# Kernel optimization log

Hardware: AMD Instinct MI355X
Metric: run time of the kernel (lower is better)

The kernel has to match this reference:

```python
import jax, jax.numpy as jnp
import numpy as np
from jax import lax

B, T, I, H = 64, 2048, 64, 256


def setup_inputs() -> dict:
    key = jax.random.key(0)
    ks = jax.random.split(key, 7)
    s = 1.0 / np.sqrt(H)  # PyTorch LSTM/Linear init scale
    x = jax.random.normal(ks[0], (B, T, I), dtype=jnp.float32)
    W_ih = jax.random.uniform(ks[1], (4 * H, I), minval=-s, maxval=s, dtype=jnp.float32)
    W_hh = jax.random.uniform(ks[2], (4 * H, H), minval=-s, maxval=s, dtype=jnp.float32)
    b_ih = jax.random.uniform(ks[3], (4 * H,), minval=-s, maxval=s, dtype=jnp.float32)
    b_hh = jax.random.uniform(ks[4], (4 * H,), minval=-s, maxval=s, dtype=jnp.float32)
    W_o = jax.random.uniform(ks[5], (1, H), minval=-s, maxval=s, dtype=jnp.float32)
    b_o = jax.random.uniform(ks[6], (1,), minval=-s, maxval=s, dtype=jnp.float32)
    return {"x": x, "W_ih": W_ih, "W_hh": W_hh, "b_ih": b_ih, "b_hh": b_hh, "W_o": W_o, "b_o": b_o}


def _lstm(x, W_ih, W_hh, b_ih, b_hh):
    # x: [B, T, I]. PyTorch gate order: i, f, g, o.
    Bn, Tn, _ = x.shape
    Hn = W_hh.shape[1]
    # Precompute input contribution for all timesteps (one big GEMM).
    gx = jnp.einsum('bti,gi->btg', x, W_ih) + b_ih + b_hh  # [B, T, 4H]

    def step(carry, gxt):
        h, c = carry
        gates = gxt + h @ W_hh.T  # [B, 4H]
        i, f, g, o = jnp.split(gates, 4, axis=-1)
        c = jax.nn.sigmoid(f) * c + jax.nn.sigmoid(i) * jnp.tanh(g)
        h = jax.nn.sigmoid(o) * jnp.tanh(c)
        return (h, c), h

    h0 = jnp.zeros((Bn, Hn), x.dtype)
    (_, _), hs = lax.scan(step, (h0, h0), jnp.swapaxes(gx, 0, 1))  # hs: [T, B, H]
    return jnp.swapaxes(hs, 0, 1)  # [B, T, H]


def reference(x, W_ih, W_hh, b_ih, b_hh, W_o, b_o):
    hs = _lstm(x, W_ih, W_hh, b_ih, b_hh)          # [B, T, H]
    return hs @ W_o.T + b_o                         # [B, T, 1]
```

## Files before the change

kernel.cpp:

```cpp
#include <hip/hip_runtime.h>
#include <hip/hip_fp16.h>

#define B_  64
#define T_  2048
#define I_  64
#define H_  256
#define G4_ 1024

typedef _Float16 h2v __attribute__((ext_vector_type(2)));

__device__ __forceinline__ float fdot2(uint32_t a, uint32_t b, float c) {
#if __has_builtin(__builtin_amdgcn_fdot2)
    return __builtin_amdgcn_fdot2(__builtin_bit_cast(h2v, a), __builtin_bit_cast(h2v, b), c, false);
#else
    h2v ha = __builtin_bit_cast(h2v, a), hb = __builtin_bit_cast(h2v, b);
    return c + (float)ha.x * (float)hb.x + (float)ha.y * (float)hb.y;
#endif
}

__device__ __forceinline__ ushort f2h(float v) {
    return __builtin_bit_cast(ushort, (_Float16)v);
}
__device__ __forceinline__ float h2f(ushort v) {
    return (float)__builtin_bit_cast(_Float16, v);
}

__global__ void repack_kernel(const float* __restrict__ Whh, ushort* __restrict__ wpk) {
    int o  = blockIdx.x * 256 + threadIdx.x;
    int j  = o & 7;
    int h  = (o >> 3) & 255;
    int kc = (o >> 11) & 31;
    int g  = o >> 16;
    float v = Whh[(g * 256 + h) * 256 + kc * 8 + j];
    wpk[o] = f2h(v);
}

__global__ __launch_bounds__(256) void gx_kernel(
    const float* __restrict__ x, const float* __restrict__ Wih,
    const float* __restrict__ bih, const float* __restrict__ bhh,
    ushort* __restrict__ gx2, int t0, int TCc) {

    __shared__ uint32_t xsp[32][32];
    const int bt0 = blockIdx.x * 32;
    const int gq  = blockIdx.y;
    const int row = gq * 256 + threadIdx.x;

    for (int i = threadIdx.x; i < 512; i += 256) {
        int r  = i >> 4, c4 = i & 15;
        int bt = bt0 + r;
        int b  = bt / TCc;
        int tl = bt - b * TCc;
        float4 v = *(const float4*)(&x[(((size_t)b * T_) + t0 + tl) * I_ + c4 * 4]);
        xsp[r][c4 * 2 + 0] = (uint32_t)f2h(v.x) | ((uint32_t)f2h(v.y) << 16);
        xsp[r][c4 * 2 + 1] = (uint32_t)f2h(v.z) | ((uint32_t)f2h(v.w) << 16);
    }
    __syncthreads();

    uint32_t wp[32];
#pragma unroll
    for (int k = 0; k < 32; ++k) {
        float a = Wih[row * I_ + 2 * k];
        float b = Wih[row * I_ + 2 * k + 1];
        wp[k] = (uint32_t)f2h(a) | ((uint32_t)f2h(b) << 16);
    }
    const float bias = bih[row] + bhh[row];

    for (int i = 0; i < 32; ++i) {
        float acc = bias;
#pragma unroll
        for (int k4 = 0; k4 < 8; ++k4) {
            uint4 xq = *(const uint4*)(&xsp[i][k4 * 4]);
            acc = fdot2(wp[k4 * 4 + 0], xq.x, acc);
            acc = fdot2(wp[k4 * 4 + 1], xq.y, acc);
            acc = fdot2(wp[k4 * 4 + 2], xq.z, acc);
            acc = fdot2(wp[k4 * 4 + 3], xq.w, acc);
        }
        gx2[((size_t)(bt0 + i) * 256 + threadIdx.x) * 4 + gq] = f2h(acc);
    }
}

__global__ __launch_bounds__(512, 1)
void lstm_kernel(
    const ushort* __restrict__ wpk, const ushort* __restrict__ gx2,
    ushort* __restrict__ hbuf,
    float* __restrict__ state,
    int TCc, int t0, int first) {

    __shared__ __align__(16) ushort wg4[14 * 2 * 256 * 8];
    __shared__ __align__(16) ushort hs[256];
    __shared__ __align__(16) float pex[256][4];

    const int tid   = threadIdx.x;
    const int hd    = tid & 255;
    const int q     = tid >> 8;
    const int kbase = q << 4;
    const int b     = blockIdx.x;
    const bool q0   = (q == 0);

    uint32_t wi[64], wf[64], wg[64];
#pragma unroll
    for (int k = 0; k < 16; ++k) {
        uint4 v = *(const uint4*)(wpk + (size_t)(0 * 32 + kbase + k) * 2048 + hd * 8);
        wi[k * 4 + 0] = v.x; wi[k * 4 + 1] = v.y; wi[k * 4 + 2] = v.z; wi[k * 4 + 3] = v.w;
    }
#pragma unroll
    for (int k = 0; k < 16; ++k) {
        uint4 v = *(const uint4*)(wpk + (size_t)(1 * 32 + kbase + k) * 2048 + hd * 8);
        wf[k * 4 + 0] = v.x; wf[k * 4 + 1] = v.y; wf[k * 4 + 2] = v.z; wf[k * 4 + 3] = v.w;
    }
#pragma unroll
    for (int k = 0; k < 16; ++k) {
        uint4 v = *(const uint4*)(wpk + (size_t)(2 * 32 + kbase + k) * 2048 + hd * 8);
        wg[k * 4 + 0] = v.x; wg[k * 4 + 1] = v.y; wg[k * 4 + 2] = v.z; wg[k * 4 + 3] = v.w;
    }
#pragma unroll
    for (int k = 0; k < 14; ++k) {
        uint4 v = *(const uint4*)(wpk + (size_t)(3 * 32 + kbase + k) * 2048 + hd * 8);
        *(uint4*)(wg4 + ((k * 2 + q) * 256 + hd) * 8) = v;
    }
    uint32_t wo_r[8];
#pragma unroll
    for (int k = 0; k < 2; ++k) {
        uint4 v = *(const uint4*)(wpk + (size_t)(3 * 32 + kbase + 14 + k) * 2048 + hd * 8);
        wo_r[k * 4 + 0] = v.x; wo_r[k * 4 + 1] = v.y; wo_r[k * 4 + 2] = v.z; wo_r[k * 4 + 3] = v.w;
    }

    float c = 0.f, h = 0.f;
    if (q0) {
        if (!first) {
            c = state[b * H_ + hd];
            h = state[B_ * H_ + b * H_ + hd];
        }
        hs[hd] = f2h(h);
    }
    __syncthreads();

    const ushort* gxb = gx2 + (size_t)b * TCc * G4_;
    ushort* hb = hbuf + (size_t)b * T_ * H_ + (size_t)t0 * H_;

    ushort4 cg;
    if (q0) cg = *(const ushort4*)(gxb + (size_t)0 * G4_ + hd * 4);

    for (int tl = 0; tl < TCc; ++tl) {
        ushort4 ng;
        if (q0) {
            const int tn = (tl + 1 < TCc) ? tl + 1 : tl;
            ng = *(const ushort4*)(gxb + (size_t)tn * G4_ + hd * 4);
        }

        float ai = 0.f, af = 0.f, agv = 0.f, ao = 0.f;

#pragma unroll
        for (int k = 0; k < 14; ++k) {
            const int kc = kbase + k;
            uint4 hq = *(const uint4*)(hs + kc * 8);
            uint4 wo = *(const uint4*)(wg4 + ((k * 2 + q) * 256 + hd) * 8);
            ai  = fdot2(wi[k * 4 + 0], hq.x, ai);
            ai  = fdot2(wi[k * 4 + 1], hq.y, ai);
            ai  = fdot2(wi[k * 4 + 2], hq.z, ai);
            ai  = fdot2(wi[k * 4 + 3], hq.w, ai);
            af  = fdot2(wf[k * 4 + 0], hq.x, af);
            af  = fdot2(wf[k * 4 + 1], hq.y, af);
            af  = fdot2(wf[k * 4 + 2], hq.z, af);
            af  = fdot2(wf[k * 4 + 3], hq.w, af);
            agv = fdot2(wg[k * 4 + 0], hq.x, agv);
            agv = fdot2(wg[k * 4 + 1], hq.y, agv);
            agv = fdot2(wg[k * 4 + 2], hq.z, agv);
            agv = fdot2(wg[k * 4 + 3], hq.w, agv);
            ao  = fdot2(wo.x, hq.x, ao);
            ao  = fdot2(wo.y, hq.y, ao);
            ao  = fdot2(wo.z, hq.z, ao);
            ao  = fdot2(wo.w, hq.w, ao);
        }
#pragma unroll
        for (int k = 14; k < 16; ++k) {
            const int kc = kbase + k;
            const int r  = (k - 14) * 4;
            uint4 hq = *(const uint4*)(hs + kc * 8);
            ai  = fdot2(wi[k * 4 + 0], hq.x, ai);
            ai  = fdot2(wi[k * 4 + 1], hq.y, ai);
            ai  = fdot2(wi[k * 4 + 2], hq.z, ai);
            ai  = fdot2(wi[k * 4 + 3], hq.w, ai);
            af  = fdot2(wf[k * 4 + 0], hq.x, af);
            af  = fdot2(wf[k * 4 + 1], hq.y, af);
            af  = fdot2(wf[k * 4 + 2], hq.z, af);
            af  = fdot2(wf[k * 4 + 3], hq.w, af);
            agv = fdot2(wg[k * 4 + 0], hq.x, agv);
            agv = fdot2(wg[k * 4 + 1], hq.y, agv);
            agv = fdot2(wg[k * 4 + 2], hq.z, agv);
            agv = fdot2(wg[k * 4 + 3], hq.w, agv);
            ao  = fdot2(wo_r[r + 0], hq.x, ao);
            ao  = fdot2(wo_r[r + 1], hq.y, ao);
            ao  = fdot2(wo_r[r + 2], hq.z, ao);
            ao  = fdot2(wo_r[r + 3], hq.w, ao);
        }

        if (!q0) {
            float4 p; p.x = ai; p.y = af; p.z = agv; p.w = ao;
            *(float4*)(&pex[hd][0]) = p;
        }
        __syncthreads();

        if (q0) {
            float4 px = *(const float4*)(&pex[hd][0]);
            ai += px.x; af += px.y; agv += px.z; ao += px.w;

            ai += h2f(cg.x); af += h2f(cg.y); agv += h2f(cg.z); ao += h2f(cg.w);

            float si = __builtin_amdgcn_rcpf(1.f + __expf(-ai));
            float sf = __builtin_amdgcn_rcpf(1.f + __expf(-af));
            float so = __builtin_amdgcn_rcpf(1.f + __expf(-ao));
            float eg = __expf(2.f * agv);
            float tg = (eg - 1.f) * __builtin_amdgcn_rcpf(eg + 1.f);
            c = sf * c + si * tg;
            float ec = __expf(2.f * c);
            float tc = (ec - 1.f) * __builtin_amdgcn_rcpf(ec + 1.f);
            h = so * tc;

            ushort hh = f2h(h);
            hs[hd] = hh;
            hb[(size_t)tl * H_ + hd] = hh;
            cg = ng;
        }
        __syncthreads();
    }

    if (q0) {
        state[b * H_ + hd]           = c;
        state[B_ * H_ + b * H_ + hd] = h;
    }
}

__global__ __launch_bounds__(256) void proj_kernel(
    const ushort* __restrict__ hbuf, const float* __restrict__ Wo,
    const float* __restrict__ bo, float* __restrict__ out) {

    const int lane = threadIdx.x & 63;
    const int wid  = blockIdx.x * 4 + (threadIdx.x >> 6);
    const int nw   = gridDim.x * 4;
    const int rows = B_ * T_;

    float4 w = *(const float4*)(Wo + lane * 4);
    const float bov = bo[0];

    for (int r = wid; r < rows; r += nw) {
        const ushort* hp = hbuf + (size_t)r * H_ + lane * 4;
        ushort4 u = *(const ushort4*)hp;
        float p = h2f(u.x) * w.x + h2f(u.y) * w.y + h2f(u.z) * w.z + h2f(u.w) * w.w;
#pragma unroll
        for (int m = 1; m < 64; m <<= 1) p += __shfl_xor(p, m, 64);
        if (lane == 0) out[r] = p + bov;
    }
}

extern "C" void kernel_launch(void* const* d_in, const int* in_sizes, int n_in,
                              void* d_out, int out_size, void* d_ws, size_t ws_size,
                              hipStream_t stream) {
    const float* x   = (const float*)d_in[0];
    const float* Wih = (const float*)d_in[1];
    const float* Whh = (const float*)d_in[2];
    const float* bih = (const float*)d_in[3];
    const float* bhh = (const float*)d_in[4];
    const float* Wo  = (const float*)d_in[5];
    const float* bo  = (const float*)d_in[6];
    float* out = (float*)d_out;

    char* ws = (char*)d_ws;
    ushort* wpk   = (ushort*)ws;
    float*  state = (float*)(ws + 512 * 1024);
    ushort* hbuf  = (ushort*)(ws + 640 * 1024);
    const size_t hbuf_bytes = (size_t)B_ * T_ * H_ * 2;
    char*   dyn   = ws + 640 * 1024 + hbuf_bytes;

    size_t fixed = 640 * 1024 + hbuf_bytes;
    size_t avail = (ws_size > fixed) ? ws_size - fixed : 0;
    long long tcmax = (long long)(avail / ((size_t)B_ * G4_ * 2));
    int TC = (tcmax > 512) ? 512 : (int)tcmax;
    TC &= ~63;
    if (TC < 64) TC = 64;

    repack_kernel<<<1024, 256, 0, stream>>>(Whh, wpk);

    for (int t0 = 0; t0 < T_; t0 += TC) {
        int TCc = (T_ - t0 < TC) ? (T_ - t0) : TC;
        ushort* gxb = (ushort*)dyn;
        dim3 g1((B_ * TCc) / 32, 4);
        gx_kernel<<<g1, 256, 0, stream>>>(x, Wih, bih, bhh, gxb, t0, TCc);
        lstm_kernel<<<B_, 512, 0, stream>>>(wpk, gxb, hbuf, state, TCc, t0, t0 == 0 ? 1 : 0);
    }
    proj_kernel<<<512, 256, 0, stream>>>(hbuf, Wo, bo, out);
    (void)in_sizes; (void)n_in; (void)out_size;
}
```

Before: 3.123 ms.

## Split LSTM gates across two workgroups per batch with global-memory flag handshake

Each batch row is now handled by two workgroups (128 total), each computing two of the four gate matvecs with weights fully in registers, which removes the shared-memory weight tile for the fourth gate. Partial gate sums are exchanged every timestep through global memory, using double-buffered slots and release/acquire flag spinning between the paired blocks. This halves per-step FMA work per block and spreads the recurrence over more CUs. In exchange it adds a cross-CU round trip through L2 on every step and relies on both paired blocks being co-resident, otherwise the spin-wait can deadlock.

New measurement: 10.12 ms. 224% more time.

```diff
diff --git a/kernel.cpp b/kernel.cpp
--- a/kernel.cpp
+++ b/kernel.cpp
@@ -84,45 +84,33 @@
     const ushort* __restrict__ wpk, const ushort* __restrict__ gx2,
     ushort* __restrict__ hbuf,
     float* __restrict__ state,
+    unsigned* __restrict__ flags,
+    unsigned long long* __restrict__ parts,
     int TCc, int t0, int first) {
 
-    __shared__ __align__(16) ushort wg4[14 * 2 * 256 * 8];
     __shared__ __align__(16) ushort hs[256];
-    __shared__ __align__(16) float pex[256][4];
+    __shared__ __align__(16) float pex[256][2];
 
     const int tid   = threadIdx.x;
     const int hd    = tid & 255;
     const int q     = tid >> 8;
     const int kbase = q << 4;
-    const int b     = blockIdx.x;
+    const int role  = blockIdx.x >> 6;
+    const int b     = blockIdx.x & 63;
     const bool q0   = (q == 0);
-
-    uint32_t wi[64], wf[64], wg[64];
+    const int glo   = role * 2;
+    const int ghi   = role * 2 + 1;
+
+    uint32_t wa[64], wb[64];
 #pragma unroll
     for (int k = 0; k < 16; ++k) {
-        uint4 v = *(const uint4*)(wpk + (size_t)(0 * 32 + kbase + k) * 2048 + hd * 8);
-        wi[k * 4 + 0] = v.x; wi[k * 4 + 1] = v.y; wi[k * 4 + 2] = v.z; wi[k * 4 + 3] = v.w;
+        uint4 v = *(const uint4*)(wpk + (size_t)(glo * 32 + kbase + k) * 2048 + hd * 8);
+        wa[k * 4 + 0] = v.x; wa[k * 4 + 1] = v.y; wa[k * 4 + 2] = v.z; wa[k * 4 + 3] = v.w;
     }
 #pragma unroll
     for (int k = 0; k < 16; ++k) {
-        uint4 v = *(const uint4*)(wpk + (size_t)(1 * 32 + kbase + k) * 2048 + hd * 8);
-        wf[k * 4 + 0] = v.x; wf[k * 4 + 1] = v.y; wf[k * 4 + 2] = v.z; wf[k * 4 + 3] = v.w;
-    }
-#pragma unroll
-    for (int k = 0; k < 16; ++k) {
-        uint4 v = *(const uint4*)(wpk + (size_t)(2 * 32 + kbase + k) * 2048 + hd * 8);
-        wg[k * 4 + 0] = v.x; wg[k * 4 + 1] = v.y; wg[k * 4 + 2] = v.z; wg[k * 4 + 3] = v.w;
-    }
-#pragma unroll
-    for (int k = 0; k < 14; ++k) {
-        uint4 v = *(const uint4*)(wpk + (size_t)(3 * 32 + kbase + k) * 2048 + hd * 8);
-        *(uint4*)(wg4 + ((k * 2 + q) * 256 + hd) * 8) = v;
-    }
-    uint32_t wo_r[8];
-#pragma unroll
-    for (int k = 0; k < 2; ++k) {
-        uint4 v = *(const uint4*)(wpk + (size_t)(3 * 32 + kbase + 14 + k) * 2048 + hd * 8);
-        wo_r[k * 4 + 0] = v.x; wo_r[k * 4 + 1] = v.y; wo_r[k * 4 + 2] = v.z; wo_r[k * 4 + 3] = v.w;
+        uint4 v = *(const uint4*)(wpk + (size_t)(ghi * 32 + kbase + k) * 2048 + hd * 8);
+        wb[k * 4 + 0] = v.x; wb[k * 4 + 1] = v.y; wb[k * 4 + 2] = v.z; wb[k * 4 + 3] = v.w;
     }
 
     float c = 0.f, h = 0.f;
@@ -138,79 +126,75 @@
     const ushort* gxb = gx2 + (size_t)b * TCc * G4_;
     ushort* hb = hbuf + (size_t)b * T_ * H_ + (size_t)t0 * H_;
 
+    unsigned long long* pme = parts + (((size_t)role * 2) * 64 + b) * 256;
+    unsigned long long* pot = parts + (((size_t)(role ^ 1) * 2) * 64 + b) * 256;
+    unsigned* fme = flags + role * 64 + b;
+    unsigned* fot = flags + (role ^ 1) * 64 + b;
+
     ushort4 cg;
     if (q0) cg = *(const ushort4*)(gxb + (size_t)0 * G4_ + hd * 4);
 
     for (int tl = 0; tl < TCc; ++tl) {
+        const unsigned want = (unsigned)(t0 + tl + 1);
+        const int par = (t0 + tl) & 1;
+
         ushort4 ng;
         if (q0) {
             const int tn = (tl + 1 < TCc) ? tl + 1 : tl;
             ng = *(const ushort4*)(gxb + (size_t)tn * G4_ + hd * 4);
         }
 
-        float ai = 0.f, af = 0.f, agv = 0.f, ao = 0.f;
-
-#pragma unroll
-        for (int k = 0; k < 14; ++k) {
+        float a0 = 0.f, a1 = 0.f;
+#pragma unroll
+        for (int k = 0; k < 16; ++k) {
             const int kc = kbase + k;
             uint4 hq = *(const uint4*)(hs + kc * 8);
-            uint4 wo = *(const uint4*)(wg4 + ((k * 2 + q) * 256 + hd) * 8);
-            ai  = fdot2(wi[k * 4 + 0], hq.x, ai);
-            ai  = fdot2(wi[k * 4 + 1], hq.y, ai);
-            ai  = fdot2(wi[k * 4 + 2], hq.z, ai);
-            ai  = fdot2(wi[k * 4 + 3], hq.w, ai);
-            af  = fdot2(wf[k * 4 + 0], hq.x, af);
-            af  = fdot2(wf[k * 4 + 1], hq.y, af);
-            af  = fdot2(wf[k * 4 + 2], hq.z, af);
-            af  = fdot2(wf[k * 4 + 3], hq.w, af);
-            agv = fdot2(wg[k * 4 + 0], hq.x, agv);
-            agv = fdot2(wg[k * 4 + 1], hq.y, agv);
-            agv = fdot2(wg[k * 4 + 2], hq.z, agv);
-            agv = fdot2(wg[k * 4 + 3], hq.w, agv);
-            ao  = fdot2(wo.x, hq.x, ao);
-            ao  = fdot2(wo.y, hq.y, ao);
-            ao  = fdot2(wo.z, hq.z, ao);
-            ao  = fdot2(wo.w, hq.w, ao);
-        }
-#pragma unroll
-        for (int k = 14; k < 16; ++k) {
-            const int kc = kbase + k;
-            const int r  = (k - 14) * 4;
-            uint4 hq = *(const uint4*)(hs + kc * 8);
-            ai  = fdot2(wi[k * 4 + 0], hq.x, ai);
-            ai  = fdot2(wi[k * 4 + 1], hq.y, ai);
-            ai  = fdot2(wi[k * 4 + 2], hq.z, ai);
-            ai  = fdot2(wi[k * 4 + 3], hq.w, ai);
-            af  = fdot2(wf[k * 4 + 0], hq.x, af);
-            af  = fdot2(wf[k * 4 + 1], hq.y, af);
-            af  = fdot2(wf[k * 4 + 2], hq.z, af);
-            af  = fdot2(wf[k * 4 + 3], hq.w, af);
-            agv = fdot2(wg[k * 4 + 0], hq.x, agv);
-            agv = fdot2(wg[k * 4 + 1], hq.y, agv);
-            agv = fdot2(wg[k * 4 + 2], hq.z, agv);
-            agv = fdot2(wg[k * 4 + 3], hq.w, agv);
-            ao  = fdot2(wo_r[r + 0], hq.x, ao);
-            ao  = fdot2(wo_r[r + 1], hq.y, ao);
-            ao  = fdot2(wo_r[r + 2], hq.z, ao);
-            ao  = fdot2(wo_r[r + 3], hq.w, ao);
-        }
-
-        if (!q0) {
-            float4 p; p.x = ai; p.y = af; p.z = agv; p.w = ao;
-            *(float4*)(&pex[hd][0]) = p;
-        }
+            a0 = fdot2(wa[k * 4 + 0], hq.x, a0);
+            a0 = fdot2(wa[k * 4 + 1], hq.y, a0);
+            a0 = fdot2(wa[k * 4 + 2], hq.z, a0);
+            a0 = fdot2(wa[k * 4 + 3], hq.w, a0);
+            a1 = fdot2(wb[k * 4 + 0], hq.x, a1);
+            a1 = fdot2(wb[k * 4 + 1], hq.y, a1);
+            a1 = fdot2(wb[k * 4 + 2], hq.z, a1);
+            a1 = fdot2(wb[k * 4 + 3], hq.w, a1);
+        }
+
+        if (!q0) { pex[hd][0] = a0; pex[hd][1] = a1; }
         __syncthreads();
 
         if (q0) {
-            float4 px = *(const float4*)(&pex[hd][0]);
-            ai += px.x; af += px.y; agv += px.z; ao += px.w;
-
-            ai += h2f(cg.x); af += h2f(cg.y); agv += h2f(cg.z); ao += h2f(cg.w);
+            a0 += pex[hd][0];
+            a1 += pex[hd][1];
+            unsigned long long pk =
+                (unsigned long long)__float_as_uint(a0) |
+                ((unsigned long long)__float_as_uint(a1) << 32);
+            __hip_atomic_store(&pme[par * 16384 + hd], pk,
+                               __ATOMIC_RELAXED, __HIP_MEMORY_SCOPE_AGENT);
+        }
+        __syncthreads();
+
+        if (tid == 0) {
+            __hip_atomic_store(fme, want, __ATOMIC_RELEASE, __HIP_MEMORY_SCOPE_AGENT);
+            while (__hip_atomic_load(fot, __ATOMIC_ACQUIRE, __HIP_MEMORY_SCOPE_AGENT) < want) {}
+        }
+        __syncthreads();
+
+        if (q0) {
+            unsigned long long pk =
+                __hip_atomic_load(&pot[par * 16384 + hd],
+                                  __ATOMIC_RELAXED, __HIP_MEMORY_SCOPE_AGENT);
+            float p0 = __uint_as_float((unsigned)pk);
+            float p1 = __uint_as_float((unsigned)(pk >> 32));
+            float ai, af, ag, ao;
+            if (role == 0) { ai = a0; af = a1; ag = p0; ao = p1; }
+            else           { ag = a0; ao = a1; ai = p0; af = p1; }
+
+            ai += h2f(cg.x); af += h2f(cg.y); ag += h2f(cg.z); ao += h2f(cg.w);
 
             float si = __builtin_amdgcn_rcpf(1.f + __expf(-ai));
             float sf = __builtin_amdgcn_rcpf(1.f + __expf(-af));
             float so = __builtin_amdgcn_rcpf(1.f + __expf(-ao));
-            float eg = __expf(2.f * agv);
+            float eg = __expf(2.f * ag);
             float tg = (eg - 1.f) * __builtin_amdgcn_rcpf(eg + 1.f);
             c = sf * c + si * tg;
             float ec = __expf(2.f * c);
@@ -219,13 +203,13 @@
 
             ushort hh = f2h(h);
             hs[hd] = hh;
-            hb[(size_t)tl * H_ + hd] = hh;
+            if (role == 0) hb[(size_t)tl * H_ + hd] = hh;
             cg = ng;
         }
         __syncthreads();
     }
 
-    if (q0) {
+    if (q0 && role == 0) {
         state[b * H_ + hd]           = c;
         state[B_ * H_ + b * H_ + hd] = h;
     }
@@ -266,19 +250,23 @@
     float* out = (float*)d_out;
 
     char* ws = (char*)d_ws;
-    ushort* wpk   = (ushort*)ws;
-    float*  state = (float*)(ws + 512 * 1024);
-    ushort* hbuf  = (ushort*)(ws + 640 * 1024);
+    ushort*   wpk   = (ushort*)ws;
+    float*    state = (float*)(ws + 512 * 1024);
+    unsigned* flags = (unsigned*)(ws + 640 * 1024);
+    unsigned long long* parts =
+        (unsigned long long*)(ws + 644 * 1024);
+    ushort*   hbuf  = (ushort*)(ws + 2692 * 1024);
     const size_t hbuf_bytes = (size_t)B_ * T_ * H_ * 2;
-    char*   dyn   = ws + 640 * 1024 + hbuf_bytes;
-
-    size_t fixed = 640 * 1024 + hbuf_bytes;
+    char*     dyn   = ws + 2692 * 1024 + hbuf_bytes;
+
+    size_t fixed = 2692 * 1024 + hbuf_bytes;
     size_t avail = (ws_size > fixed) ? ws_size - fixed : 0;
     long long tcmax = (long long)(avail / ((size_t)B_ * G4_ * 2));
     int TC = (tcmax > 512) ? 512 : (int)tcmax;
     TC &= ~63;
     if (TC < 64) TC = 64;
 
+    hipMemsetAsync(flags, 0, 4096, stream);
     repack_kernel<<<1024, 256, 0, stream>>>(Whh, wpk);
 
     for (int t0 = 0; t0 < T_; t0 += TC) {
@@ -286,7 +274,8 @@
         ushort* gxb = (ushort*)dyn;
         dim3 g1((B_ * TCc) / 32, 4);
         gx_kernel<<<g1, 256, 0, stream>>>(x, Wih, bih, bhh, gxb, t0, TCc);
-        lstm_kernel<<<B_, 512, 0, stream>>>(wpk, gxb, hbuf, state, TCc, t0, t0 == 0 ? 1 : 0);
+        lstm_kernel<<<128, 512, 0, stream>>>(wpk, gxb, hbuf, state, flags, parts,
+                                             TCc, t0, t0 == 0 ? 1 : 0);
     }
     proj_kernel<<<512, 256, 0, stream>>>(hbuf, Wo, bo, out);
     (void)in_sizes; (void)n_in; (void)out_size;
```
